# Kernel tuning notes

Measured on AMD Instinct MI355X. Metric: run time of the kernel, lower is better.

The kernel has to match this reference:

```python
import jax, jax.numpy as jnp
import numpy as np

LOG_2PI = float(np.log(2.0 * np.pi))


def kde_self_log_prob(X, sigma):
    """log prob of each row of X under a KDE whose components are all rows of X.

    Matches tfd.MixtureSameFamily(Categorical(uniform), MVNDiag(loc=X, scale=sigma)):
      log p(q) = logsumexp_i [ -0.5*||q - X_i||^2/sigma^2 - d*log(sigma) - d/2*log(2pi) ] - log(N)
    """
    n, d = X.shape
    sq = jnp.sum(X * X, axis=1)  # [N]
    # pairwise squared distances [N, N]; clamp tiny negatives from cancellation
    d2 = jnp.maximum(sq[:, None] + sq[None, :] - 2.0 * (X @ X.T), 0.0)
    log_comp = -0.5 * d2 / (sigma * sigma) - d * jnp.log(sigma) - 0.5 * d * LOG_2PI
    return jax.nn.logsumexp(log_comp, axis=1) - jnp.log(jnp.asarray(n, X.dtype))


def setup_inputs() -> dict:
    key = jax.random.key(0)
    kx, ky = jax.random.split(key)
    N, D = 8192, 128
    latent_x = jax.random.normal(kx, (N, D), dtype=jnp.float32)
    latent_y = jax.random.normal(ky, (N, D), dtype=jnp.float32)
    # learned bandwidth parameters (tf.Variable scalars, init 1.0)
    sigma_joint = jnp.float32(1.0)
    sigma_x = jnp.float32(1.0)
    sigma_y = jnp.float32(1.0)
    return {"latent_x": latent_x, "latent_y": latent_y,
            "sigma_joint": sigma_joint, "sigma_x": sigma_x, "sigma_y": sigma_y}


def reference(latent_x, latent_y, sigma_joint, sigma_x, sigma_y):
    latent_joint = jnp.concatenate([latent_x, latent_y], axis=1)  # [N, 2d]
    lp_joint = kde_self_log_prob(latent_joint, sigma_joint)  # [N]
    lp_x = kde_self_log_prob(latent_x, sigma_x)              # [N]
    lp_y = kde_self_log_prob(latent_y, sigma_y)              # [N]
    I_xy = jnp.exp(lp_joint) * (lp_joint - (lp_x + lp_y))
    return -jnp.sum(I_xy)
```

## Files before the change

kernel.cpp:

```cpp
#include <hip/hip_runtime.h>
#include <hip/hip_bf16.h>
#include <math.h>

#define NROW 8192
#define DD   128

#define V8BLK  256
#define V8NBLK 1024
#define NRANKV8 8128

#define NT   64
#define TS   128
#define NPAIR 2080
#define FBLOCK 512

#define LOG_2PI 1.8378770664093453f
#define L2E     1.4426950408889634f
#define FP_SCALE 1099511627776.0

typedef __attribute__((ext_vector_type(8))) short bf16x8;
typedef __attribute__((ext_vector_type(4))) float f32x4;

#define SQX_B 0
#define SQY_B 32768
#define BSUM_B 65536
#define XB_B  65792
#define YB_B  (XB_B + NROW*DD*2)
#define TS_B  (YB_B + NROW*DD*2)
#define COLV8_B  TS_B
#define ROWSV8_B (COLV8_B + NRANKV8*192*4)
#define PS_B     (ROWSV8_B + 2048*192*4)
#define V8_NEED  (PS_B + 128*8*192*4)
#define ACC_B TS_B

__device__ __forceinline__ unsigned short f2bf(float f) {
    unsigned int x = __float_as_uint(f);
    unsigned int r = (x + 0x7fffu + ((x >> 16) & 1u)) >> 16;
    return (unsigned short)r;
}
__device__ __forceinline__ float fexp2(float x) { return __builtin_amdgcn_exp2f(x); }
__device__ __forceinline__ int rank_v8(int I, int J) {
    return I * 127 - (I * (I - 1)) / 2 + (J - I - 1);
}

template <bool PRE>
__global__ void sq_kernel(const float* __restrict__ X, const float* __restrict__ Y,
                          float* __restrict__ sqx, float* __restrict__ sqy,
                          unsigned short* __restrict__ XB, unsigned short* __restrict__ YB) {
    int tid  = threadIdx.x;
    int rowg = blockIdx.x * 8 + (tid >> 5);
    int lane = tid & 31;
    bool isX = rowg < NROW;
    const float* src = isX ? (X + (size_t)rowg * DD) : (Y + (size_t)(rowg - NROW) * DD);
    float4 v = reinterpret_cast<const float4*>(src)[lane];
    if (PRE) {
        unsigned int w0 = (unsigned int)f2bf(v.x) | ((unsigned int)f2bf(v.y) << 16);
        unsigned int w1 = (unsigned int)f2bf(v.z) | ((unsigned int)f2bf(v.w) << 16);
        unsigned short* dst = (isX ? XB + (size_t)rowg * DD
                                   : YB + (size_t)(rowg - NROW) * DD) + lane * 4;
        uint2 pk; pk.x = w0; pk.y = w1;
        *reinterpret_cast<uint2*>(dst) = pk;
    }
    float s = v.x * v.x + v.y * v.y + v.z * v.z + v.w * v.w;
#pragma unroll
    for (int m = 16; m; m >>= 1) s += __shfl_xor(s, m, 64);
    if (lane == 0) { if (isX) sqx[rowg] = s; else sqy[rowg - NROW] = s; }
}

template <bool SAME, bool DIAG>
__device__ __forceinline__ void combine_v8(const f32x4 (&ax)[4], const f32x4 (&ay)[4],
                                           const float* __restrict__ sqi0,
                                           const float* __restrict__ sqi1,
                                           float bxp, float byp,
                                           float cx2, float cy2, float m2cx, float m2cy,
                                           float rx, float ry,
                                           float (&prow)[4][4][3], float (&pcol)[3],
                                           int lane, int wq) {
    const int coll = wq * 16 + (lane & 15);
#pragma unroll
    for (int rf = 0; rf < 4; ++rf) {
        const int rb = rf * 16 + ((lane >> 4) << 2);
        f32x4 sixv = *reinterpret_cast<const f32x4*>(&sqi0[rb]);
        f32x4 siyv = *reinterpret_cast<const f32x4*>(&sqi1[rb]);
#pragma unroll
        for (int reg = 0; reg < 4; ++reg) {
            float tx = fmaf(ax[rf][reg], m2cx, fmaf(cx2, sixv[reg], bxp));
            float ty = fmaf(ay[rf][reg], m2cy, fmaf(cy2, siyv[reg], byp));
            float ex = fexp2(tx);
            float ey = fexp2(ty);
            float ej = SAME ? (ex * ey) : fexp2(fmaf(tx, rx, ty * ry));
            if (DIAG) {
                bool dg = (rb + reg) == coll;
                ex = dg ? 1.f : ex;  ey = dg ? 1.f : ey;  ej = dg ? 1.f : ej;
            }
            prow[rf][reg][0] += ex; prow[rf][reg][1] += ey; prow[rf][reg][2] += ej;
            pcol[0] += ex;          pcol[1] += ey;          pcol[2] += ej;
        }
    }
}

__launch_bounds__(V8BLK, 1)
__global__ void kde_v8(const unsigned short* __restrict__ XB,
                       const unsigned short* __restrict__ YB,
                       const float* __restrict__ sjp, const float* __restrict__ sxp,
                       const float* __restrict__ syp,
                       const float* __restrict__ sqx, const float* __restrict__ sqy,
                       float* __restrict__ COL, float* __restrict__ ROWS) {
    __shared__ unsigned short A[2][64][DD];
    __shared__ float sqi[2][64];
    __shared__ float rowred[4][64][3];

    const int tid  = threadIdx.x;
    const int lane = tid & 63;
    const int wq   = tid >> 6;

    const int bid = blockIdx.x;
    const int cch = bid & 15;
    const int p   = bid >> 4;
    const int t0  = (129 * cch) >> 4;
    const int t1  = (129 * (cch + 1)) >> 4;

    const float sxv = *sxp, syv = *syp, sjv = *sjp;
    const float cx2 = -0.5f * L2E / (sxv * sxv);
    const float cy2 = -0.5f * L2E / (syv * syv);
    const float cj2 = -0.5f * L2E / (sjv * sjv);
    const bool  same = (cx2 == cy2) && (cy2 == cj2);
    const float m2cx = -2.f * cx2, m2cy = -2.f * cy2;
    const float rx = cj2 / cx2, ry = cj2 / cy2;

    float prow[4][4][3];
#pragma unroll
    for (int a = 0; a < 4; ++a)
#pragma unroll
        for (int b = 0; b < 4; ++b)
#pragma unroll
            for (int c = 0; c < 3; ++c) prow[a][b][c] = 0.f;

    int  curI = -1;
    bool wrote0 = false, wrote1 = false;

    for (int m = t0; m < t1; ++m) {
        int I, J;
        if (m < 128 - p) { I = p;       J = p + m; }
        else             { I = 127 - p; J = m - 1; }
        const bool diag = (I == J);
        const int j0 = J * 64;

        if (I != curI) {
            const bool hadPrev = (curI >= 0);
            const int prevWhich = (curI == p) ? 0 : 1;
            __syncthreads();
            if (hadPrev) {
#pragma unroll
                for (int rf = 0; rf < 4; ++rf)
#pragma unroll
                    for (int reg = 0; reg < 4; ++reg)
#pragma unroll
                        for (int ch = 0; ch < 3; ++ch) {
                            float v = prow[rf][reg][ch];
                            v += __shfl_xor(v, 1, 64);
                            v += __shfl_xor(v, 2, 64);
                            v += __shfl_xor(v, 4, 64);
                            v += __shfl_xor(v, 8, 64);
                            if ((lane & 15) == 0)
                                rowred[wq][rf * 16 + ((lane >> 4) << 2) + reg][ch] = v;
                            prow[rf][reg][ch] = 0.f;
                        }
            }
            {
                int mat   = wq >> 1;
                int rband = (wq & 1) * 32;
                const unsigned short* gb = (mat ? YB : XB) + (size_t)(I * 64) * DD;
#pragma unroll
                for (int i = 0; i < 8; ++i) {
                    int row = rband + i * 4 + (lane >> 4);
                    uint4 v = *reinterpret_cast<const uint4*>(gb + (size_t)row * DD + (lane & 15) * 8);
                    int sl = (lane & 15) ^ (row & 7);
                    *reinterpret_cast<uint4*>(&A[mat][row][sl * 8]) = v;
                }
            }
            if (tid < 128) sqi[tid >> 6][tid & 63] = ((tid < 64) ? sqx : sqy)[I * 64 + (tid & 63)];
            __syncthreads();
            if (hadPrev && tid < 192) {
                int ch = tid >> 6, row = tid & 63;
                size_t slot = ((size_t)(p * 16 + cch) * 2 + prevWhich);
                ROWS[(slot * 3 + ch) * 64 + row] = rowred[0][row][ch] + rowred[1][row][ch]
                                                 + rowred[2][row][ch] + rowred[3][row][ch];
            }
            if (hadPrev) { if (prevWhich == 0) wrote0 = true; else wrote1 = true; }
            curI = I;
        }

        const int colg = j0 + wq * 16 + (lane & 15);
        const float bxp = cx2 * sqx[colg];
        const float byp = cy2 * sqy[colg];

        f32x4 ax[4], ay[4];
#pragma unroll
        for (int rf = 0; rf < 4; ++rf) {
            ax[rf] = (f32x4){0.f, 0.f, 0.f, 0.f};
            ay[rf] = (f32x4){0.f, 0.f, 0.f, 0.f};
        }
#pragma unroll 2
        for (int kk = 0; kk < 4; ++kk) {
            bf16x8 bfx, bfy, afx[4], afy[4];
            {
                size_t off = (size_t)colg * DD + kk * 32 + (lane >> 4) * 8;
                bfx = *reinterpret_cast<const bf16x8*>(XB + off);
                bfy = *reinterpret_cast<const bf16x8*>(YB + off);
            }
#pragma unroll
            for (int rf = 0; rf < 4; ++rf) {
                int r  = rf * 16 + (lane & 15);
                int sl = (kk * 4 + (lane >> 4)) ^ (r & 7);
                afx[rf] = *reinterpret_cast<const bf16x8*>(&A[0][r][sl * 8]);
                afy[rf] = *reinterpret_cast<const bf16x8*>(&A[1][r][sl * 8]);
            }
#pragma unroll
            for (int rf = 0; rf < 4; ++rf) {
                ax[rf] = __builtin_amdgcn_mfma_f32_16x16x32_bf16(afx[rf], bfx, ax[rf], 0, 0, 0);
                ay[rf] = __builtin_amdgcn_mfma_f32_16x16x32_bf16(afy[rf], bfy, ay[rf], 0, 0, 0);
            }
        }

        float pcol[3] = {0.f, 0.f, 0.f};
        if (same) { if (diag) combine_v8<true , true >(ax, ay, &sqi[0][0], &sqi[1][0], bxp, byp, cx2, cy2, m2cx, m2cy, rx, ry, prow, pcol, lane, wq);
                    else      combine_v8<true , false>(ax, ay, &sqi[0][0], &sqi[1][0], bxp, byp, cx2, cy2, m2cx, m2cy, rx, ry, prow, pcol, lane, wq); }
        else      { if (diag) combine_v8<false, true >(ax, ay, &sqi[0][0], &sqi[1][0], bxp, byp, cx2, cy2, m2cx, m2cy, rx, ry, prow, pcol, lane, wq);
                    else      combine_v8<false, false>(ax, ay, &sqi[0][0], &sqi[1][0], bxp, byp, cx2, cy2, m2cx, m2cy, rx, ry, prow, pcol, lane, wq); }

        if (!diag) {
            int rank = rank_v8(I, J);
#pragma unroll
            for (int ch = 0; ch < 3; ++ch) {
                float v = pcol[ch];
                v += __shfl_xor(v, 16, 64);
                v += __shfl_xor(v, 32, 64);
                if (lane < 16)
                    COL[((size_t)rank * 3 + ch) * 64 + wq * 16 + lane] = v;
            }
        }
    }

    __syncthreads();
#pragma unroll
    for (int rf = 0; rf < 4; ++rf)
#pragma unroll
        for (int reg = 0; reg < 4; ++reg)
#pragma unroll
            for (int ch = 0; ch < 3; ++ch) {
                float v = prow[rf][reg][ch];
                v += __shfl_xor(v, 1, 64);
                v += __shfl_xor(v, 2, 64);
                v += __shfl_xor(v, 4, 64);
                v += __shfl_xor(v, 8, 64);
                if ((lane & 15) == 0)
                    rowred[wq][rf * 16 + ((lane >> 4) << 2) + reg][ch] = v;
            }
    __syncthreads();
    {
        const int lastWhich = (curI == p) ? 0 : 1;
        if (tid < 192) {
            int ch = tid >> 6, row = tid & 63;
            size_t slot = ((size_t)(p * 16 + cch) * 2 + lastWhich);
            ROWS[(slot * 3 + ch) * 64 + row] = rowred[0][row][ch] + rowred[1][row][ch]
                                             + rowred[2][row][ch] + rowred[3][row][ch];
        }
        if (lastWhich == 0) wrote0 = true; else wrote1 = true;
    }
    if (!wrote0 && tid < 192) {
        int ch = tid >> 6, row = tid & 63;
        ROWS[(((size_t)(p * 16 + cch) * 2 + 0) * 3 + ch) * 64 + row] = 0.f;
    }
    if (!wrote1 && tid < 192) {
        int ch = tid >> 6, row = tid & 63;
        ROWS[(((size_t)(p * 16 + cch) * 2 + 1) * 3 + ch) * 64 + row] = 0.f;
    }
}

__global__ void colsum_v8(const float* __restrict__ COL, float* __restrict__ PS) {
    const int J = blockIdx.x;
    const int s = blockIdx.y;
    const int t = threadIdx.x;
    const int i0 = (J * s) >> 3;
    const int i1 = (J * (s + 1)) >> 3;
    float v = 0.f;
    for (int I = i0; I < i1; ++I)
        v += COL[(size_t)rank_v8(I, J) * 192 + t];
    PS[((size_t)J * 8 + s) * 192 + t] = v;
}

__global__ void lp_v8(const float* __restrict__ sjp, const float* __restrict__ sxp,
                      const float* __restrict__ syp,
                      const float* __restrict__ PS, const float* __restrict__ ROWS,
                      float* __restrict__ bsum) {
    int b = blockIdx.x;
    int t = threadIdx.x;
    int r = b * 128 + t;
    int Ib = r >> 6;
    int c  = r & 63;
    float S0 = 0.f, S1 = 0.f, S2 = 0.f;
    {
        int p = (Ib < 64) ? Ib : 127 - Ib;
        int which = (Ib < 64) ? 0 : 1;
        for (int ch4 = 0; ch4 < 16; ++ch4) {
            size_t slot = ((size_t)(p * 16 + ch4) * 2 + which) * 3;
            S0 += ROWS[(slot + 0) * 64 + c];
            S1 += ROWS[(slot + 1) * 64 + c];
            S2 += ROWS[(slot + 2) * 64 + c];
        }
    }
    for (int s = 0; s < 8; ++s) {
        size_t base = ((size_t)Ib * 8 + s) * 192 + c;
        S0 += PS[base];
        S1 += PS[base + 64];
        S2 += PS[base + 128];
    }
    float sx = *sxp, sy = *syp, sj = *sjp;
    float logN = logf((float)NROW);
    float lpx = logf(S0) - (float)DD * logf(sx) - 0.5f * (float)DD * LOG_2PI - logN;
    float lpy = logf(S1) - (float)DD * logf(sy) - 0.5f * (float)DD * LOG_2PI - logN;
    float lpj = logf(S2) - 2.0f * (float)DD * logf(sj) - (float)DD * LOG_2PI - logN;
    float I_ = expf(lpj) * (lpj - lpx - lpy);
#pragma unroll
    for (int m = 1; m < 64; m <<= 1) I_ += __shfl_xor(I_, m, 64);
    __shared__ float w0s[2];
    if ((t & 63) == 0) w0s[t >> 6] = I_;
    __syncthreads();
    if (t == 0) bsum[b] = w0s[0] + w0s[1];
}

__global__ void final_reduce(const float* __restrict__ bsum, float* __restrict__ out) {
    int t = threadIdx.x;
    float v = bsum[t];
#pragma unroll
    for (int m = 1; m < 64; m <<= 1) v += __shfl_xor(v, m, 64);
    if (t == 0) out[0] = -v;
}

template <bool SAME>
__device__ __forceinline__ void fb_combine(const f32x4 (&ax)[4][2], const f32x4 (&ay)[4][2],
                                           const float (&sq)[4][TS],
                                           float (&rowred)[4][TS][3], float (&colred)[2][TS][3],
                                           int wr, int wc, int lane,
                                           float cx2, float cy2, float cj2) {
    float pcol[2][3] = {{0.f,0.f,0.f},{0.f,0.f,0.f}};
#pragma unroll
    for (int rf = 0; rf < 4; ++rf) {
        float prow[4][3] = {{0.f,0.f,0.f},{0.f,0.f,0.f},{0.f,0.f,0.f},{0.f,0.f,0.f}};
        float sxi[4], syi[4];
#pragma unroll
        for (int reg = 0; reg < 4; ++reg) {
            int row = wr*64 + rf*16 + ((lane>>4)<<2) + reg;
            sxi[reg] = sq[0][row]; syi[reg] = sq[1][row];
        }
#pragma unroll
        for (int cf = 0; cf < 2; ++cf) {
            int col = wc*32 + cf*16 + (lane & 15);
            float qx = sq[2][col], qy = sq[3][col];
#pragma unroll
            for (int reg = 0; reg < 4; ++reg) {
                float gx = ax[rf][cf][reg], gy = ay[rf][cf][reg];
                float d2x = fmaxf(fmaf(-2.f, gx, sxi[reg] + qx), 0.f);
                float d2y = fmaxf(fmaf(-2.f, gy, syi[reg] + qy), 0.f);
                float ex = fexp2(d2x * cx2);
                float ey = fexp2(d2y * cy2);
                float ej = SAME ? (ex * ey) : fexp2(fmaf(d2y, cj2, d2x * cj2));
                prow[reg][0] += ex; prow[reg][1] += ey; prow[reg][2] += ej;
                pcol[cf][0]  += ex; pcol[cf][1]  += ey; pcol[cf][2]  += ej;
            }
        }
#pragma unroll
        for (int reg = 0; reg < 4; ++reg)
#pragma unroll
            for (int ch = 0; ch < 3; ++ch) {
                float v = prow[reg][ch];
                v += __shfl_xor(v, 1, 64); v += __shfl_xor(v, 2, 64);
                v += __shfl_xor(v, 4, 64); v += __shfl_xor(v, 8, 64);
                if ((lane & 15) == 0)
                    rowred[wc][wr*64 + rf*16 + ((lane>>4)<<2) + reg][ch] = v;
            }
    }
#pragma unroll
    for (int cf = 0; cf < 2; ++cf)
#pragma unroll
        for (int ch = 0; ch < 3; ++ch) {
            float v = pcol[cf][ch];
            v += __shfl_xor(v, 16, 64); v += __shfl_xor(v, 32, 64);
            if (lane < 16) colred[wr][wc*32 + cf*16 + lane][ch] = v;
        }
}

__launch_bounds__(FBLOCK)
__global__ void kde_fb(const float* __restrict__ X, const float* __restrict__ Y,
                       const float* __restrict__ sjp, const float* __restrict__ sxp,
                       const float* __restrict__ syp,
                       unsigned long long* __restrict__ acc,
                       const float* __restrict__ sqx, const float* __restrict__ sqy) {
    __shared__ unsigned short T[4][TS][DD];
    __shared__ float sq[4][TS];
    __shared__ float rowred[4][TS][3];
    __shared__ float colred[2][TS][3];

    const int tid  = threadIdx.x;
    const int lane = tid & 63;
    const int wid  = tid >> 6;
    const int wr   = wid >> 2;
    const int wc   = wid & 3;

    int b = (blockIdx.x & 7) * (NPAIR / 8) + (blockIdx.x >> 3);
    int ti = 0, rem = b;
    while (rem >= NT - ti) { rem -= NT - ti; ++ti; }
    int tj = ti + rem;
    const int i0 = ti * TS, j0 = tj * TS;

    const float sxv = *sxp, syv = *syp, sjv = *sjp;
    const float cx2 = -0.5f * L2E / (sxv * sxv);
    const float cy2 = -0.5f * L2E / (syv * syv);
    const float cj2 = -0.5f * L2E / (sjv * sjv);
    const bool samesig = (cx2 == cy2) && (cy2 == cj2);

    for (int c = tid; c < 8192; c += FBLOCK) {
        int t = c >> 11, row = (c >> 4) & 127, col8 = c & 15;
        const float* base =
            (t == 0) ? X + (size_t)i0 * DD : (t == 1) ? Y + (size_t)i0 * DD :
            (t == 2) ? X + (size_t)j0 * DD : Y + (size_t)j0 * DD;
        const float4* s4 = reinterpret_cast<const float4*>(base + row * DD + col8 * 8);
        float4 a = s4[0], bb = s4[1];
        unsigned int w0 = (unsigned int)f2bf(a.x)  | ((unsigned int)f2bf(a.y)  << 16);
        unsigned int w1 = (unsigned int)f2bf(a.z)  | ((unsigned int)f2bf(a.w)  << 16);
        unsigned int w2 = (unsigned int)f2bf(bb.x) | ((unsigned int)f2bf(bb.y) << 16);
        unsigned int w3 = (unsigned int)f2bf(bb.z) | ((unsigned int)f2bf(bb.w) << 16);
        uint4 pk = make_uint4(w0, w1, w2, w3);
        int sl = (col8 ^ (row & 7)) << 3;
        *reinterpret_cast<uint4*>(&T[t][row][sl]) = pk;
    }
    {
        int t = tid >> 7, r = tid & 127;
        const float* s = (t == 0) ? sqx + i0 : (t == 1) ? sqy + i0
                       : (t == 2) ? sqx + j0 : sqy + j0;
        sq[t][r] = s[r];
    }
    __syncthreads();

    f32x4 ax[4][2], ay[4][2];
#pragma unroll
    for (int rf = 0; rf < 4; ++rf)
#pragma unroll
        for (int cf = 0; cf < 2; ++cf) {
            ax[rf][cf] = (f32x4){0.f,0.f,0.f,0.f};
            ay[rf][cf] = (f32x4){0.f,0.f,0.f,0.f};
        }
#pragma unroll
    for (int kk = 0; kk < 4; ++kk) {
        const int k0 = kk * 4 + (lane >> 4);
        bf16x8 afx[4], afy[4], bfx[2], bfy[2];
#pragma unroll
        for (int rf = 0; rf < 4; ++rf) {
            int r  = wr * 64 + rf * 16 + (lane & 15);
            int sl = (k0 ^ (r & 7)) << 3;
            afx[rf] = *reinterpret_cast<const bf16x8*>(&T[0][r][sl]);
            afy[rf] = *reinterpret_cast<const bf16x8*>(&T[1][r][sl]);
        }
#pragma unroll
        for (int cf = 0; cf < 2; ++cf) {
            int r  = wc * 32 + cf * 16 + (lane & 15);
            int sl = (k0 ^ (r & 7)) << 3;
            bfx[cf] = *reinterpret_cast<const bf16x8*>(&T[2][r][sl]);
            bfy[cf] = *reinterpret_cast<const bf16x8*>(&T[3][r][sl]);
        }
#pragma unroll
        for (int rf = 0; rf < 4; ++rf)
#pragma unroll
            for (int cf = 0; cf < 2; ++cf) {
                ax[rf][cf] = __builtin_amdgcn_mfma_f32_16x16x32_bf16(afx[rf], bfx[cf], ax[rf][cf], 0, 0, 0);
                ay[rf][cf] = __builtin_amdgcn_mfma_f32_16x16x32_bf16(afy[rf], bfy[cf], ay[rf][cf], 0, 0, 0);
            }
    }

    if (samesig) fb_combine<true >(ax, ay, sq, rowred, colred, wr, wc, lane, cx2, cy2, cj2);
    else         fb_combine<false>(ax, ay, sq, rowred, colred, wr, wc, lane, cx2, cy2, cj2);
    __syncthreads();

    if (tid < TS) {
        int r = tid;
#pragma unroll
        for (int ch = 0; ch < 3; ++ch) {
            float v = rowred[0][r][ch] + rowred[1][r][ch] + rowred[2][r][ch] + rowred[3][r][ch];
            atomicAdd(&acc[(size_t)(i0 + r) * 3 + ch],
                      (unsigned long long)(long long)((double)v * FP_SCALE));
        }
    } else if (tid < 2 * TS && ti != tj) {
        int r = tid - TS;
#pragma unroll
        for (int ch = 0; ch < 3; ++ch) {
            float v = colred[0][r][ch] + colred[1][r][ch];
            atomicAdd(&acc[(size_t)(j0 + r) * 3 + ch],
                      (unsigned long long)(long long)((double)v * FP_SCALE));
        }
    }
}

__global__ void lp_fb(const float* __restrict__ sjp, const float* __restrict__ sxp,
                      const float* __restrict__ syp,
                      const unsigned long long* __restrict__ acc,
                      float* __restrict__ bsum) {
    int b = blockIdx.x, t = threadIdx.x;
    size_t row = (size_t)b * 128 + t;
    const double INV = 1.0 / FP_SCALE;
    float S0 = (float)((double)acc[row * 3 + 0] * INV);
    float S1 = (float)((double)acc[row * 3 + 1] * INV);
    float S2 = (float)((double)acc[row * 3 + 2] * INV);
    float sx = *sxp, sy = *syp, sj = *sjp;
    float logN = logf((float)NROW);
    float lpx = logf(S0) - (float)DD * logf(sx) - 0.5f * (float)DD * LOG_2PI - logN;
    float lpy = logf(S1) - (float)DD * logf(sy) - 0.5f * (float)DD * LOG_2PI - logN;
    float lpj = logf(S2) - 2.0f * (float)DD * logf(sj) - (float)DD * LOG_2PI - logN;
    float I = expf(lpj) * (lpj - lpx - lpy);
#pragma unroll
    for (int m = 1; m < 64; m <<= 1) I += __shfl_xor(I, m, 64);
    __shared__ float w0[2];
    if ((t & 63) == 0) w0[t >> 6] = I;
    __syncthreads();
    if (t == 0) bsum[b] = w0[0] + w0[1];
}

extern "C" void kernel_launch(void* const* d_in, const int* in_sizes, int n_in,
                              void* d_out, int out_size, void* d_ws, size_t ws_size,
                              hipStream_t stream) {
    (void)in_sizes; (void)n_in; (void)out_size;
    const float* X  = (const float*)d_in[0];
    const float* Y  = (const float*)d_in[1];
    const float* sj = (const float*)d_in[2];
    const float* sx = (const float*)d_in[3];
    const float* sy = (const float*)d_in[4];
    float* out = (float*)d_out;
    char*  w   = (char*)d_ws;

    float* SQX  = (float*)(w + SQX_B);
    float* SQY  = (float*)(w + SQY_B);
    float* BSUM = (float*)(w + BSUM_B);
    unsigned short* XB = (unsigned short*)(w + XB_B);
    unsigned short* YB = (unsigned short*)(w + YB_B);

    if (ws_size >= (size_t)V8_NEED) {
        float* COLS = (float*)(w + COLV8_B);
        float* ROWS = (float*)(w + ROWSV8_B);
        float* PS   = (float*)(w + PS_B);
        sq_kernel<true ><<<dim3(2048), dim3(256), 0, stream>>>(X, Y, SQX, SQY, XB, YB);
        kde_v8<<<dim3(V8NBLK), dim3(V8BLK), 0, stream>>>(XB, YB, sj, sx, sy, SQX, SQY, COLS, ROWS);
        colsum_v8<<<dim3(128, 8), dim3(192), 0, stream>>>(COLS, PS);
        lp_v8<<<dim3(64), dim3(128), 0, stream>>>(sj, sx, sy, PS, ROWS, BSUM);
    } else {
        unsigned long long* ACC = (unsigned long long*)(w + ACC_B);
        hipMemsetAsync(w + ACC_B, 0, NROW * 3 * sizeof(unsigned long long), stream);
        sq_kernel<false><<<dim3(2048), dim3(256), 0, stream>>>(X, Y, SQX, SQY, XB, YB);
        kde_fb<<<dim3(NPAIR), dim3(FBLOCK), 0, stream>>>(X, Y, sj, sx, sy, ACC, SQX, SQY);
        lp_fb<<<dim3(64), dim3(128), 0, stream>>>(sj, sx, sy, ACC, BSUM);
    }
    final_reduce<<<dim3(1), dim3(64), 0, stream>>>(BSUM, out);
}
```

Measured before the change: 89.51 us.

## Use 512-thread blocks with two wave groups sharing each staged row tile

The KDE kernel now launches half as many blocks with twice the threads. Two groups of four waves process alternating column tiles against the same shared-memory row tile, and the tile walk is split into at most two bands per block. Each staged A tile is therefore reused across more column tiles, and the block count per CU changes. In exchange, tiles are spread over fewer, larger blocks, an odd tile count leaves one wave group idle, and the row reduction now sums eight wave partials.

```diff
diff --git a/kernel.cpp b/kernel.cpp
--- a/kernel.cpp
+++ b/kernel.cpp
@@ -5,8 +5,8 @@
 #define NROW 8192
 #define DD   128
 
-#define V8BLK  256
-#define V8NBLK 1024
+#define V12BLK  512
+#define V12NBLK 512
 #define NRANKV8 8128
 
 #define NT   64
@@ -75,8 +75,8 @@
                                            float cx2, float cy2, float m2cx, float m2cy,
                                            float rx, float ry,
                                            float (&prow)[4][4][3], float (&pcol)[3],
-                                           int lane, int wq) {
-    const int coll = wq * 16 + (lane & 15);
+                                           int lane, int wql) {
+    const int coll = wql * 16 + (lane & 15);
 #pragma unroll
     for (int rf = 0; rf < 4; ++rf) {
         const int rb = rf * 16 + ((lane >> 4) << 2);
@@ -99,26 +99,29 @@
     }
 }
 
-__launch_bounds__(V8BLK, 1)
-__global__ void kde_v8(const unsigned short* __restrict__ XB,
-                       const unsigned short* __restrict__ YB,
-                       const float* __restrict__ sjp, const float* __restrict__ sxp,
-                       const float* __restrict__ syp,
-                       const float* __restrict__ sqx, const float* __restrict__ sqy,
-                       float* __restrict__ COL, float* __restrict__ ROWS) {
+__launch_bounds__(V12BLK, 1)
+__global__ void kde_v12(const unsigned short* __restrict__ XB,
+                        const unsigned short* __restrict__ YB,
+                        const float* __restrict__ sjp, const float* __restrict__ sxp,
+                        const float* __restrict__ syp,
+                        const float* __restrict__ sqx, const float* __restrict__ sqy,
+                        float* __restrict__ COL, float* __restrict__ ROWS) {
     __shared__ unsigned short A[2][64][DD];
     __shared__ float sqi[2][64];
-    __shared__ float rowred[4][64][3];
+    __shared__ float rowred[8][64][3];
 
     const int tid  = threadIdx.x;
     const int lane = tid & 63;
     const int wq   = tid >> 6;
+    const int wg   = wq >> 2;
+    const int wql  = wq & 3;
 
     const int bid = blockIdx.x;
-    const int cch = bid & 15;
-    const int p   = bid >> 4;
-    const int t0  = (129 * cch) >> 4;
-    const int t1  = (129 * (cch + 1)) >> 4;
+    const int cch = bid & 7;
+    const int p   = bid >> 3;
+    const int t0  = (129 * cch) >> 3;
+    const int t1  = (129 * (cch + 1)) >> 3;
+    const int nJA = 128 - p;
 
     const float sxv = *sxp, syv = *syp, sjv = *sjp;
     const float cx2 = -0.5f * L2E / (sxv * sxv);
@@ -136,108 +139,117 @@
 #pragma unroll
             for (int c = 0; c < 3; ++c) prow[a][b][c] = 0.f;
 
-    int  curI = -1;
+    int  prevWhich = -1;
     bool wrote0 = false, wrote1 = false;
 
-    for (int m = t0; m < t1; ++m) {
-        int I, J;
-        if (m < 128 - p) { I = p;       J = p + m; }
-        else             { I = 127 - p; J = m - 1; }
-        const bool diag = (I == J);
-        const int j0 = J * 64;
-
-        if (I != curI) {
-            const bool hadPrev = (curI >= 0);
-            const int prevWhich = (curI == p) ? 0 : 1;
-            __syncthreads();
-            if (hadPrev) {
-#pragma unroll
-                for (int rf = 0; rf < 4; ++rf)
-#pragma unroll
-                    for (int reg = 0; reg < 4; ++reg)
-#pragma unroll
-                        for (int ch = 0; ch < 3; ++ch) {
-                            float v = prow[rf][reg][ch];
-                            v += __shfl_xor(v, 1, 64);
-                            v += __shfl_xor(v, 2, 64);
-                            v += __shfl_xor(v, 4, 64);
-                            v += __shfl_xor(v, 8, 64);
-                            if ((lane & 15) == 0)
-                                rowred[wq][rf * 16 + ((lane >> 4) << 2) + reg][ch] = v;
-                            prow[rf][reg][ch] = 0.f;
-                        }
-            }
-            {
-                int mat   = wq >> 1;
-                int rband = (wq & 1) * 32;
-                const unsigned short* gb = (mat ? YB : XB) + (size_t)(I * 64) * DD;
-#pragma unroll
-                for (int i = 0; i < 8; ++i) {
-                    int row = rband + i * 4 + (lane >> 4);
-                    uint4 v = *reinterpret_cast<const uint4*>(gb + (size_t)row * DD + (lane & 15) * 8);
-                    int sl = (lane & 15) ^ (row & 7);
-                    *reinterpret_cast<uint4*>(&A[mat][row][sl * 8]) = v;
+    const int e1 = (t1 < nJA) ? t1 : nJA;
+    const int s0 = (t0 > nJA) ? t0 : nJA;
+
+    for (int band = 0; band < 2; ++band) {
+        int I, Jf, cnt;
+        if (band == 0) { I = p;       Jf = p + t0;  cnt = e1 - t0; }
+        else           { I = 127 - p; Jf = s0 - 1;  cnt = t1 - s0; }
+        if (cnt <= 0) continue;
+
+        __syncthreads();
+        if (prevWhich >= 0) {
+#pragma unroll
+            for (int rf = 0; rf < 4; ++rf)
+#pragma unroll
+                for (int reg = 0; reg < 4; ++reg)
+#pragma unroll
+                    for (int ch = 0; ch < 3; ++ch) {
+                        float v = prow[rf][reg][ch];
+                        v += __shfl_xor(v, 1, 64);
+                        v += __shfl_xor(v, 2, 64);
+                        v += __shfl_xor(v, 4, 64);
+                        v += __shfl_xor(v, 8, 64);
+                        if ((lane & 15) == 0)
+                            rowred[wq][rf * 16 + ((lane >> 4) << 2) + reg][ch] = v;
+                        prow[rf][reg][ch] = 0.f;
+                    }
+        }
+        {
+            int mat = wq >> 2;
+            int g   = tid & 255;
+            const unsigned short* gb = (mat ? YB : XB) + (size_t)(I * 64) * DD;
+#pragma unroll
+            for (int i = 0; i < 4; ++i) {
+                int e    = g + i * 256;
+                int row  = e >> 4;
+                int col8 = e & 15;
+                uint4 v = *reinterpret_cast<const uint4*>(gb + (size_t)row * DD + col8 * 8);
+                int sl = col8 ^ (row & 7);
+                *reinterpret_cast<uint4*>(&A[mat][row][sl * 8]) = v;
+            }
+        }
+        if (tid < 128) sqi[tid >> 6][tid & 63] = ((tid < 64) ? sqx : sqy)[I * 64 + (tid & 63)];
+        __syncthreads();
+        if (prevWhich >= 0 && tid < 192) {
+            int ch = tid >> 6, row = tid & 63;
+            size_t slot = ((size_t)(p * 8 + cch) * 2 + prevWhich);
+            float v = 0.f;
+#pragma unroll
+            for (int w = 0; w < 8; ++w) v += rowred[w][row][ch];
+            ROWS[(slot * 3 + ch) * 64 + row] = v;
+        }
+        if (prevWhich == 0) wrote0 = true; else if (prevWhich == 1) wrote1 = true;
+        prevWhich = (I == p) ? 0 : 1;
+
+        for (int s = 0; s < cnt; s += 2) {
+            const int  so    = s + wg;
+            const bool valid = so < cnt;
+            if (!valid) continue;
+            const int J    = Jf + so;
+            const bool diag = (I == J);
+            const int colg = J * 64 + wql * 16 + (lane & 15);
+            const float bxp = cx2 * sqx[colg];
+            const float byp = cy2 * sqy[colg];
+
+            f32x4 ax[4], ay[4];
+#pragma unroll
+            for (int rf = 0; rf < 4; ++rf) {
+                ax[rf] = (f32x4){0.f, 0.f, 0.f, 0.f};
+                ay[rf] = (f32x4){0.f, 0.f, 0.f, 0.f};
+            }
+#pragma unroll 2
+            for (int kk = 0; kk < 4; ++kk) {
+                bf16x8 bfx, bfy, afx[4], afy[4];
+                {
+                    size_t off = (size_t)colg * DD + kk * 32 + (lane >> 4) * 8;
+                    bfx = *reinterpret_cast<const bf16x8*>(XB + off);
+                    bfy = *reinterpret_cast<const bf16x8*>(YB + off);
                 }
-            }
-            if (tid < 128) sqi[tid >> 6][tid & 63] = ((tid < 64) ? sqx : sqy)[I * 64 + (tid & 63)];
-            __syncthreads();
-            if (hadPrev && tid < 192) {
-                int ch = tid >> 6, row = tid & 63;
-                size_t slot = ((size_t)(p * 16 + cch) * 2 + prevWhich);
-                ROWS[(slot * 3 + ch) * 64 + row] = rowred[0][row][ch] + rowred[1][row][ch]
-                                                 + rowred[2][row][ch] + rowred[3][row][ch];
-            }
-            if (hadPrev) { if (prevWhich == 0) wrote0 = true; else wrote1 = true; }
-            curI = I;
-        }
-
-        const int colg = j0 + wq * 16 + (lane & 15);
-        const float bxp = cx2 * sqx[colg];
-        const float byp = cy2 * sqy[colg];
-
-        f32x4 ax[4], ay[4];
-#pragma unroll
-        for (int rf = 0; rf < 4; ++rf) {
-            ax[rf] = (f32x4){0.f, 0.f, 0.f, 0.f};
-            ay[rf] = (f32x4){0.f, 0.f, 0.f, 0.f};
-        }
-#pragma unroll 2
-        for (int kk = 0; kk < 4; ++kk) {
-            bf16x8 bfx, bfy, afx[4], afy[4];
-            {
-                size_t off = (size_t)colg * DD + kk * 32 + (lane >> 4) * 8;
-                bfx = *reinterpret_cast<const bf16x8*>(XB + off);
-                bfy = *reinterpret_cast<const bf16x8*>(YB + off);
-            }
-#pragma unroll
-            for (int rf = 0; rf < 4; ++rf) {
-                int r  = rf * 16 + (lane & 15);
-                int sl = (kk * 4 + (lane >> 4)) ^ (r & 7);
-                afx[rf] = *reinterpret_cast<const bf16x8*>(&A[0][r][sl * 8]);
-                afy[rf] = *reinterpret_cast<const bf16x8*>(&A[1][r][sl * 8]);
-            }
-#pragma unroll
-            for (int rf = 0; rf < 4; ++rf) {
-                ax[rf] = __builtin_amdgcn_mfma_f32_16x16x32_bf16(afx[rf], bfx, ax[rf], 0, 0, 0);
-                ay[rf] = __builtin_amdgcn_mfma_f32_16x16x32_bf16(afy[rf], bfy, ay[rf], 0, 0, 0);
-            }
-        }
-
-        float pcol[3] = {0.f, 0.f, 0.f};
-        if (same) { if (diag) combine_v8<true , true >(ax, ay, &sqi[0][0], &sqi[1][0], bxp, byp, cx2, cy2, m2cx, m2cy, rx, ry, prow, pcol, lane, wq);
-                    else      combine_v8<true , false>(ax, ay, &sqi[0][0], &sqi[1][0], bxp, byp, cx2, cy2, m2cx, m2cy, rx, ry, prow, pcol, lane, wq); }
-        else      { if (diag) combine_v8<false, true >(ax, ay, &sqi[0][0], &sqi[1][0], bxp, byp, cx2, cy2, m2cx, m2cy, rx, ry, prow, pcol, lane, wq);
-                    else      combine_v8<false, false>(ax, ay, &sqi[0][0], &sqi[1][0], bxp, byp, cx2, cy2, m2cx, m2cy, rx, ry, prow, pcol, lane, wq); }
-
-        if (!diag) {
-            int rank = rank_v8(I, J);
-#pragma unroll
-            for (int ch = 0; ch < 3; ++ch) {
-                float v = pcol[ch];
-                v += __shfl_xor(v, 16, 64);
-                v += __shfl_xor(v, 32, 64);
-                if (lane < 16)
-                    COL[((size_t)rank * 3 + ch) * 64 + wq * 16 + lane] = v;
+#pragma unroll
+                for (int rf = 0; rf < 4; ++rf) {
+                    int r  = rf * 16 + (lane & 15);
+                    int sl = (kk * 4 + (lane >> 4)) ^ (r & 7);
+                    afx[rf] = *reinterpret_cast<const bf16x8*>(&A[0][r][sl * 8]);
+                    afy[rf] = *reinterpret_cast<const bf16x8*>(&A[1][r][sl * 8]);
+                }
+#pragma unroll
+                for (int rf = 0; rf < 4; ++rf) {
+                    ax[rf] = __builtin_amdgcn_mfma_f32_16x16x32_bf16(afx[rf], bfx, ax[rf], 0, 0, 0);
+                    ay[rf] = __builtin_amdgcn_mfma_f32_16x16x32_bf16(afy[rf], bfy, ay[rf], 0, 0, 0);
+                }
+            }
+
+            float pcol[3] = {0.f, 0.f, 0.f};
+            if (same) { if (diag) combine_v8<true , true >(ax, ay, &sqi[0][0], &sqi[1][0], bxp, byp, cx2, cy2, m2cx, m2cy, rx, ry, prow, pcol, lane, wql);
+                        else      combine_v8<true , false>(ax, ay, &sqi[0][0], &sqi[1][0], bxp, byp, cx2, cy2, m2cx, m2cy, rx, ry, prow, pcol, lane, wql); }
+            else      { if (diag) combine_v8<false, true >(ax, ay, &sqi[0][0], &sqi[1][0], bxp, byp, cx2, cy2, m2cx, m2cy, rx, ry, prow, pcol, lane, wql);
+                        else      combine_v8<false, false>(ax, ay, &sqi[0][0], &sqi[1][0], bxp, byp, cx2, cy2, m2cx, m2cy, rx, ry, prow, pcol, lane, wql); }
+
+            if (!diag) {
+                int rank = rank_v8(I, J);
+#pragma unroll
+                for (int ch = 0; ch < 3; ++ch) {
+                    float v = pcol[ch];
+                    v += __shfl_xor(v, 16, 64);
+                    v += __shfl_xor(v, 32, 64);
+                    if (lane < 16)
+                        COL[((size_t)rank * 3 + ch) * 64 + wql * 16 + lane] = v;
+                }
             }
         }
     }
@@ -258,23 +270,22 @@
                     rowred[wq][rf * 16 + ((lane >> 4) << 2) + reg][ch] = v;
             }
     __syncthreads();
-    {
-        const int lastWhich = (curI == p) ? 0 : 1;
-        if (tid < 192) {
-            int ch = tid >> 6, row = tid & 63;
-            size_t slot = ((size_t)(p * 16 + cch) * 2 + lastWhich);
-            ROWS[(slot * 3 + ch) * 64 + row] = rowred[0][row][ch] + rowred[1][row][ch]
-                                             + rowred[2][row][ch] + rowred[3][row][ch];
-        }
-        if (lastWhich == 0) wrote0 = true; else wrote1 = true;
-    }
+    if (tid < 192) {
+        int ch = tid >> 6, row = tid & 63;
+        size_t slot = ((size_t)(p * 8 + cch) * 2 + prevWhich);
+        float v = 0.f;
+#pragma unroll
+        for (int w = 0; w < 8; ++w) v += rowred[w][row][ch];
+        ROWS[(slot * 3 + ch) * 64 + row] = v;
+    }
+    if (prevWhich == 0) wrote0 = true; else wrote1 = true;
     if (!wrote0 && tid < 192) {
         int ch = tid >> 6, row = tid & 63;
-        ROWS[(((size_t)(p * 16 + cch) * 2 + 0) * 3 + ch) * 64 + row] = 0.f;
+        ROWS[(((size_t)(p * 8 + cch) * 2 + 0) * 3 + ch) * 64 + row] = 0.f;
     }
     if (!wrote1 && tid < 192) {
         int ch = tid >> 6, row = tid & 63;
-        ROWS[(((size_t)(p * 16 + cch) * 2 + 1) * 3 + ch) * 64 + row] = 0.f;
+        ROWS[(((size_t)(p * 8 + cch) * 2 + 1) * 3 + ch) * 64 + row] = 0.f;
     }
 }
 
@@ -290,10 +301,10 @@
     PS[((size_t)J * 8 + s) * 192 + t] = v;
 }
 
-__global__ void lp_v8(const float* __restrict__ sjp, const float* __restrict__ sxp,
-                      const float* __restrict__ syp,
-                      const float* __restrict__ PS, const float* __restrict__ ROWS,
-                      float* __restrict__ bsum) {
+__global__ void lp_v12(const float* __restrict__ sjp, const float* __restrict__ sxp,
+                       const float* __restrict__ syp,
+                       const float* __restrict__ PS, const float* __restrict__ ROWS,
+                       float* __restrict__ bsum) {
     int b = blockIdx.x;
     int t = threadIdx.x;
     int r = b * 128 + t;
@@ -303,8 +314,8 @@
     {
         int p = (Ib < 64) ? Ib : 127 - Ib;
         int which = (Ib < 64) ? 0 : 1;
-        for (int ch4 = 0; ch4 < 16; ++ch4) {
-            size_t slot = ((size_t)(p * 16 + ch4) * 2 + which) * 3;
+        for (int ch8 = 0; ch8 < 8; ++ch8) {
+            size_t slot = ((size_t)(p * 8 + ch8) * 2 + which) * 3;
             S0 += ROWS[(slot + 0) * 64 + c];
             S1 += ROWS[(slot + 1) * 64 + c];
             S2 += ROWS[(slot + 2) * 64 + c];
@@ -548,9 +559,9 @@
         float* ROWS = (float*)(w + ROWSV8_B);
         float* PS   = (float*)(w + PS_B);
         sq_kernel<true ><<<dim3(2048), dim3(256), 0, stream>>>(X, Y, SQX, SQY, XB, YB);
-        kde_v8<<<dim3(V8NBLK), dim3(V8BLK), 0, stream>>>(XB, YB, sj, sx, sy, SQX, SQY, COLS, ROWS);
+        kde_v12<<<dim3(V12NBLK), dim3(V12BLK), 0, stream>>>(XB, YB, sj, sx, sy, SQX, SQY, COLS, ROWS);
         colsum_v8<<<dim3(128, 8), dim3(192), 0, stream>>>(COLS, PS);
-        lp_v8<<<dim3(64), dim3(128), 0, stream>>>(sj, sx, sy, PS, ROWS, BSUM);
+        lp_v12<<<dim3(64), dim3(128), 0, stream>>>(sj, sx, sy, PS, ROWS, BSUM);
     } else {
         unsigned long long* ACC = (unsigned long long*)(w + ACC_B);
         hipMemsetAsync(w + ACC_B, 0, NROW * 3 * sizeof(unsigned long long), stream);
```

Result: no change. 89.38 us (-0.1%).
